# Optimization experiments

Hardware: AMD Instinct MI355X
Metric: run time of the kernel (lower is better)

## Reference

```python
import jax, jax.numpy as jnp
import numpy as np

# LLaMA-style decoder config (shrunken for reference): L layers, hidden D, H heads,
# SwiGLU width F, vocab V, LoRA rank R.
B, S, D, H, F, V, L, R = 2, 512, 1024, 16, 4096, 32000, 2, 16
DH = D // H
LORA_ALPHA = 32.0
EPS = 1e-5
ROPE_THETA = 10000.0


def setup_inputs() -> dict:
    key = jax.random.key(0)
    ks = iter(jax.random.split(key, 40))
    def n(shape, std=0.02):
        return jax.random.normal(next(ks), shape, jnp.float32) * std
    return {
        "input_ids": jax.random.randint(next(ks), (B, S), 0, V),
        "attention_mask": jnp.ones((B, S), jnp.int32),
        "embed": n((V, D)),
        "ln1": jnp.ones((L, D), jnp.float32),
        "ln2": jnp.ones((L, D), jnp.float32),
        "wq": n((L, D, D)), "aq": n((L, D, R)), "bq": n((L, R, D), 0.01),
        "wk": n((L, D, D)), "ak": n((L, D, R)), "bk": n((L, R, D), 0.01),
        "wv": n((L, D, D)), "av": n((L, D, R)), "bv": n((L, R, D), 0.01),
        "wo": n((L, D, D)), "ao": n((L, D, R)), "bo": n((L, R, D), 0.01),
        "wg": n((L, D, F)), "ag": n((L, D, R)), "bg": n((L, R, F), 0.01),
        "wu": n((L, D, F)), "au": n((L, D, R)), "bu": n((L, R, F), 0.01),
        "wd": n((L, F, D)), "ad": n((L, F, R)), "bd": n((L, R, D), 0.01),
        "final_ln": jnp.ones((D,), jnp.float32),
        "lm_head_w": n((D, V)),
        "value_w": n((D, 1)),
        "value_b": jnp.zeros((1,), jnp.float32),
    }


def _rmsnorm(x, w):
    return x * jax.lax.rsqrt(jnp.mean(x * x, axis=-1, keepdims=True) + EPS) * w


def _lin_lora(x, w, a, b):
    # base matmul + low-rank LoRA update scaled by alpha/r (dropout=eval/off)
    return x @ w + ((x @ a) @ b) * (LORA_ALPHA / R)


def _rope_cache(seq_len):
    half = DH // 2
    inv = 1.0 / (ROPE_THETA ** (jnp.arange(half, dtype=jnp.float32) / half))
    ang = jnp.arange(seq_len, dtype=jnp.float32)[:, None] * inv  # [S, half]
    ang = jnp.concatenate([ang, ang], axis=-1)                   # [S, DH]
    return jnp.cos(ang), jnp.sin(ang)


def _apply_rope(x, cos, sin):  # x: [B,S,H,DH]
    h = DH // 2
    rot = jnp.concatenate([-x[..., h:], x[..., :h]], axis=-1)
    return x * cos[None, :, None, :] + rot * sin[None, :, None, :]


def reference(input_ids, attention_mask, embed, ln1, ln2,
              wq, aq, bq, wk, ak, bk, wv, av, bv, wo, ao, bo,
              wg, ag, bg, wu, au, bu, wd, ad, bd,
              final_ln, lm_head_w, value_w, value_b):
    h = embed[input_ids]  # [B,S,D]
    cos, sin = _rope_cache(S)
    causal = jnp.tril(jnp.ones((S, S), bool))
    keep = causal[None, None, :, :] & (attention_mask[:, None, None, :] > 0)
    bias = jnp.where(keep, 0.0, -1e9)  # [B,1,S,S]
    scale = 1.0 / jnp.sqrt(jnp.float32(DH))

    for i in range(L):
        # --- self-attention block ---
        x = _rmsnorm(h, ln1[i])
        q = _lin_lora(x, wq[i], aq[i], bq[i]).reshape(B, S, H, DH)
        k = _lin_lora(x, wk[i], ak[i], bk[i]).reshape(B, S, H, DH)
        v = _lin_lora(x, wv[i], av[i], bv[i]).reshape(B, S, H, DH)
        q = _apply_rope(q, cos, sin)
        k = _apply_rope(k, cos, sin)
        scores = jnp.einsum("bqhd,bkhd->bhqk", q, k) * scale + bias
        attn = jax.nn.softmax(scores, axis=-1)
        o = jnp.einsum("bhqk,bkhd->bqhd", attn, v).reshape(B, S, D)
        h = h + _lin_lora(o, wo[i], ao[i], bo[i])
        # --- SwiGLU MLP block ---
        x = _rmsnorm(h, ln2[i])
        g = jax.nn.silu(_lin_lora(x, wg[i], ag[i], bg[i]))
        u = _lin_lora(x, wu[i], au[i], bu[i])
        h = h + _lin_lora(g * u, wd[i], ad[i], bd[i])

    h = _rmsnorm(h, final_ln)          # HF hidden_states[-1] is post final norm
    logits = h @ lm_head_w             # [B,S,V]
    values = (h @ value_w)[..., 0] + value_b[0]  # [B,S] (squeeze(-1))
    return logits, values
```

## Files before the change

kernel.cpp:

```cpp
#include <hip/hip_runtime.h>
#include <math.h>

constexpr int B = 2, S = 512, D = 1024, H = 16, F = 4096, V = 32000, L = 2, R = 16, DH = 64;
constexpr int BS = B * S;
constexpr float LORA_SCALE = 2.0f;
constexpr float EPS = 1e-5f;
constexpr int RS_QKV = 3 * D;
constexpr int RS_GU  = 2 * F;

typedef __attribute__((ext_vector_type(8))) __bf16 bf16x8;
typedef __attribute__((ext_vector_type(4))) float f32x4;

__device__ __forceinline__ unsigned short f2bf(float f) {
  unsigned u = __builtin_bit_cast(unsigned, f);
  unsigned r = (u + 0x7FFFu + ((u >> 16) & 1u)) >> 16;
  return (unsigned short)r;
}
__device__ __forceinline__ float bf2f(unsigned short us) {
  return __builtin_bit_cast(float, (unsigned)us << 16);
}
__device__ __forceinline__ void load_lds16(const void* g, void* l) {
  __builtin_amdgcn_global_load_lds((const __attribute__((address_space(1))) void*)g,
                                   (__attribute__((address_space(3))) void*)l, 16, 0, 0);
}

struct Ptr3 { const float* p[3]; };

__global__ void rope_cache_kernel(float* __restrict__ cosb, float* __restrict__ sinb) {
  int s = blockIdx.x, j = threadIdx.x;
  float inv = __expf(-(float)j * (9.210340371976184f / 32.0f));
  float ang = (float)s * inv;
  float c = cosf(ang), sn = sinf(ang);
  cosb[s * DH + j] = c;  cosb[s * DH + j + 32] = c;
  sinb[s * DH + j] = sn; sinb[s * DH + j + 32] = sn;
}

__global__ void embed_kernel(const int* __restrict__ ids, const float* __restrict__ emb,
                             float* __restrict__ h) {
  int row = blockIdx.x, t = threadIdx.x;
  int id = ids[row];
  ((float4*)(h + (size_t)row * D))[t] = ((const float4*)(emb + (size_t)id * D))[t];
}

__global__ void rmsnorm_value_kernel(const float* __restrict__ x, const float* __restrict__ w,
                                     const float* __restrict__ vw, const float* __restrict__ vb,
                                     unsigned short* __restrict__ y, float* __restrict__ values) {
  int row = blockIdx.x, t = threadIdx.x;
  float4 xv = ((const float4*)(x + (size_t)row * D))[t];
  float ss = xv.x * xv.x + xv.y * xv.y + xv.z * xv.z + xv.w * xv.w;
  __shared__ float red[256];
  red[t] = ss; __syncthreads();
  for (int s2 = 128; s2; s2 >>= 1) { if (t < s2) red[t] += red[t + s2]; __syncthreads(); }
  float rinv = rsqrtf(red[0] * (1.0f / D) + EPS);
  float4 wv = ((const float4*)w)[t];
  float4 nx;
  nx.x = xv.x * rinv * wv.x; nx.y = xv.y * rinv * wv.y;
  nx.z = xv.z * rinv * wv.z; nx.w = xv.w * rinv * wv.w;
  ushort4 o;
  o.x = f2bf(nx.x); o.y = f2bf(nx.y); o.z = f2bf(nx.z); o.w = f2bf(nx.w);
  ((ushort4*)(y + (size_t)row * D))[t] = o;
  float4 vv = ((const float4*)vw)[t];
  float vd = nx.x * vv.x + nx.y * vv.y + nx.z * vv.z + nx.w * vv.w;
  __syncthreads();
  red[t] = vd; __syncthreads();
  for (int s2 = 128; s2; s2 >>= 1) { if (t < s2) red[t] += red[t + s2]; __syncthreads(); }
  if (t == 0) values[row] = red[0] + vb[0];
}

template <int NA>
__global__ void rms_lora_kernel(const float* __restrict__ hp, const float* __restrict__ w,
                                Ptr3 ap, unsigned short* __restrict__ xbf,
                                unsigned short* __restrict__ t2e) {
  int row = blockIdx.x, t = threadIdx.x;
  int lane = t & 63;
  __shared__ float xs[D];
  __shared__ float red[256];
  float4 xv = ((const float4*)(hp + (size_t)row * D))[t];
  float ss = xv.x * xv.x + xv.y * xv.y + xv.z * xv.z + xv.w * xv.w;
  red[t] = ss; __syncthreads();
  for (int s2 = 128; s2; s2 >>= 1) { if (t < s2) red[t] += red[t + s2]; __syncthreads(); }
  float rinv = rsqrtf(red[0] * (1.0f / D) + EPS);
  float4 wv = ((const float4*)w)[t];
  float4 nx;
  nx.x = xv.x * rinv * wv.x; nx.y = xv.y * rinv * wv.y;
  nx.z = xv.z * rinv * wv.z; nx.w = xv.w * rinv * wv.w;
  xs[t * 4 + 0] = nx.x; xs[t * 4 + 1] = nx.y; xs[t * 4 + 2] = nx.z; xs[t * 4 + 3] = nx.w;
  ushort4 o;
  o.x = f2bf(nx.x); o.y = f2bf(nx.y); o.z = f2bf(nx.z); o.w = f2bf(nx.w);
  ((ushort4*)(xbf + (size_t)row * D))[t] = o;
  if (t >= NA * 16 && t < 64) t2e[(size_t)row * 64 + t] = 0;
  __syncthreads();
  int n = t & 15, g = t >> 4;
#pragma unroll
  for (int ad = 0; ad < NA; ++ad) {
    const float* a = ap.p[ad];
    float s = 0.0f;
    for (int k = g; k < D; k += 16) s = fmaf(xs[k], a[k * 16 + n], s);
    s += __shfl_xor(s, 16);
    s += __shfl_xor(s, 32);
    if (lane < 16) red[(t >> 6) * 16 + n] = s;
    __syncthreads();
    if (t < 16) t2e[(size_t)row * 64 + ad * 16 + t] =
        f2bf(LORA_SCALE * (red[t] + red[t + 16] + red[t + 32] + red[t + 48]));
    if (ad + 1 < NA) __syncthreads();
  }
}

__global__ void lora_o_kernel(const unsigned short* __restrict__ xb, const float* __restrict__ a,
                              unsigned short* __restrict__ t2e) {
  int row = blockIdx.x, t = threadIdx.x;
  int lane = t & 63;
  __shared__ float xs[D];
  __shared__ float red[64];
  for (int k = t; k < D; k += 256) xs[k] = bf2f(xb[(size_t)row * D + k]);
  if (t >= 16 && t < 64) t2e[(size_t)row * 64 + t] = 0;
  __syncthreads();
  int n = t & 15, g = t >> 4;
  float s = 0.0f;
  for (int k = g; k < D; k += 16) s = fmaf(xs[k], a[k * 16 + n], s);
  s += __shfl_xor(s, 16);
  s += __shfl_xor(s, 32);
  if (lane < 16) red[(t >> 6) * 16 + n] = s;
  __syncthreads();
  if (t < 16) t2e[(size_t)row * 64 + t] =
      f2bf(LORA_SCALE * (red[t] + red[t + 16] + red[t + 32] + red[t + 48]));
}

__global__ void silu_lora_kernel(const unsigned short* __restrict__ gub, const float* __restrict__ a,
                                 unsigned short* __restrict__ gbf, unsigned short* __restrict__ t2e) {
  int row = blockIdx.x, t = threadIdx.x;
  int lane = t & 63;
  __shared__ float xs[F];
  __shared__ float red[64];
#pragma unroll
  for (int i2 = 0; i2 < 2; ++i2) {
    int idx = i2 * 256 + t;
    uint4 gv = ((const uint4*)(gub + (size_t)row * RS_GU))[idx];
    uint4 uv = ((const uint4*)(gub + (size_t)row * RS_GU + F))[idx];
    const unsigned* gw = (const unsigned*)&gv;
    const unsigned* uw = (const unsigned*)&uv;
    unsigned short go[8];
#pragma unroll
    for (int q = 0; q < 4; ++q) {
      float g0 = bf2f((unsigned short)(gw[q] & 0xffff)), g1 = bf2f((unsigned short)(gw[q] >> 16));
      float u0 = bf2f((unsigned short)(uw[q] & 0xffff)), u1 = bf2f((unsigned short)(uw[q] >> 16));
      float r0 = g0 / (1.0f + __expf(-g0)) * u0;
      float r1 = g1 / (1.0f + __expf(-g1)) * u1;
      xs[idx * 8 + q * 2] = r0; xs[idx * 8 + q * 2 + 1] = r1;
      go[q * 2] = f2bf(r0); go[q * 2 + 1] = f2bf(r1);
    }
    *(uint4*)(gbf + (size_t)row * F + idx * 8) = *(const uint4*)go;
  }
  if (t >= 16 && t < 64) t2e[(size_t)row * 64 + t] = 0;
  __syncthreads();
  int n = t & 15, g = t >> 4;
  float s = 0.0f;
  for (int k = g; k < F; k += 16) s = fmaf(xs[k], a[k * 16 + n], s);
  s += __shfl_xor(s, 16);
  s += __shfl_xor(s, 32);
  if (lane < 16) red[(t >> 6) * 16 + n] = s;
  __syncthreads();
  if (t < 16) t2e[(size_t)row * 64 + t] =
      f2bf(LORA_SCALE * (red[t] + red[t + 16] + red[t + 32] + red[t + 48]));
}

struct BD { const float* p0; const float* p1; const float* p2;
            unsigned short* dst; int NA; int logW; int nelem; };
struct BDs { BD d[8]; };
__global__ void bext_many_kernel(BDs da) {
  int gid = blockIdx.x * 256 + threadIdx.x;
  int di = 0;
  while (gid >= da.d[di].nelem) { gid -= da.d[di].nelem; ++di; }
  const BD dd = da.d[di];
  int n = gid >> 6, kk = gid & 63;
  int W = 1 << dd.logW;
  int sel = n >> dd.logW;
  const float* bp = (sel == 0) ? dd.p0 : (sel == 1) ? dd.p1 : dd.p2;
  float v = 0.0f;
  if ((kk >> 4) == sel && sel < dd.NA)
    v = bp[(size_t)(kk & 15) * W + (n & (W - 1))];
  dd.dst[(size_t)n * 64 + kk] = f2bf(v);
}

struct TD { const float* src; unsigned short* dst; int K; int N; int nblk; };
struct TDs { TD d[15]; };
__global__ __launch_bounds__(256) void transpose_many_kernel(TDs da) {
  __shared__ unsigned short tile[64 * 264];
  int bid = blockIdx.x;
  int di = 0;
  while (bid >= da.d[di].nblk) { bid -= da.d[di].nblk; ++di; }
  const TD dd = da.d[di];
  int nbx = dd.N >> 6;
  int n0 = (bid % nbx) * 64, k0 = (bid / nbx) * 256;
  int t = threadIdx.x;
  int rr = t >> 4, c4 = (t & 15) << 2;
  float4 v[16];
#pragma unroll
  for (int i = 0; i < 16; ++i)
    v[i] = *(const float4*)(dd.src + (size_t)(k0 + i * 16 + rr) * dd.N + n0 + c4);
#pragma unroll
  for (int i = 0; i < 16; ++i) {
    int k = i * 16 + rr;
#pragma unroll
    for (int j = 0; j < 4; ++j) {
      int n = c4 + j;
      float e = (j == 0) ? v[i].x : (j == 1) ? v[i].y : (j == 2) ? v[i].z : v[i].w;
      tile[n * 264 + (k ^ ((n & 3) << 3))] = f2bf(e);
    }
  }
  __syncthreads();
#pragma unroll
  for (int i = 0; i < 8; ++i) {
    int flat = i * 256 + t;
    int n = flat >> 5, cw = flat & 31;
    int kb = (cw * 8) ^ ((n & 3) << 3);
    *(uint4*)(dd.dst + (size_t)(n0 + n) * dd.K + k0 + cw * 8) =
        *(const uint4*)(tile + n * 264 + kb);
  }
}

template <int BN, bool ACC, bool EXT, int OM>
__global__ __launch_bounds__(256) void gemm_bf16_kernel(
    const unsigned short* __restrict__ A, const unsigned short* __restrict__ Bt,
    void* __restrict__ Cp, int M, int N, int K,
    const unsigned short* __restrict__ Ae, const unsigned short* __restrict__ Be,
    const float* __restrict__ cosb, const float* __restrict__ sinb) {
  constexpr int WM = (BN == 128) ? 2 : 4;
  constexpr int RW = 128 / WM;
  constexpr int MI = RW / 16;
  constexpr int BCH = BN / 32;
  __shared__ __align__(16) unsigned short As[2][128 * 64];
  __shared__ __align__(16) unsigned short Bs[2][BN * 64];
  int t = threadIdx.x;
  int lane = t & 63, wave = t >> 6;
  int wr = (BN == 128) ? (wave >> 1) : wave;
  int wc = (BN == 128) ? (wave & 1) : 0;
  int MT = gridDim.y, NT = gridDim.x;
  int nwg = MT * NT;
  int orig = blockIdx.y * NT + blockIdx.x;
  int qq = nwg >> 3, rr8 = nwg & 7;
  int xcd = orig & 7, pos = orig >> 3;
  int wg = (xcd < rr8) ? (xcd * (qq + 1) + pos) : (rr8 * (qq + 1) + (xcd - rr8) * qq + pos);
  int m0 = (wg % MT) * 128, n0 = (wg / MT) * BN;
  int fr = lane & 15, fq = lane >> 4;
  int xorv = fr & 7;
  f32x4 acc[MI][4] = {};
  int kIters = K / 64;
  int nIters = EXT ? kIters + 1 : kIters;

  auto STAGE = [&](int it, int buf) {
    bool ext = EXT && (it == kIters);
    int k0 = it * 64;
#pragma unroll
    for (int c = 0; c < 4; ++c) {
      int i = c * 256 + t;
      int row = i >> 3, c8 = i & 7;
      int sc = (c8 ^ (row & 7)) * 8;
      const unsigned short* src = ext ? (Ae + (size_t)(m0 + row) * 64 + sc)
                                      : (A + (size_t)(m0 + row) * K + k0 + sc);
      load_lds16(src, &As[buf][i * 8]);
    }
#pragma unroll
    for (int c = 0; c < BCH; ++c) {
      int i = c * 256 + t;
      int row = i >> 3, c8 = i & 7;
      int sc = (c8 ^ (row & 7)) * 8;
      const unsigned short* src = ext ? (Be + (size_t)(n0 + row) * 64 + sc)
                                      : (Bt + (size_t)(n0 + row) * K + k0 + sc);
      load_lds16(src, &Bs[buf][i * 8]);
    }
  };

  STAGE(0, 0);
  if (nIters > 1) STAGE(1, 1);
  int cur = 0;
  for (int it = 0; it < nIters; ++it) {
    if (it + 1 < nIters) {
      if constexpr (BN == 128) asm volatile("s_waitcnt vmcnt(8)" ::: "memory");
      else                     asm volatile("s_waitcnt vmcnt(6)" ::: "memory");
    } else {
      asm volatile("s_waitcnt vmcnt(0)" ::: "memory");
    }
    __builtin_amdgcn_s_barrier();
#pragma unroll
    for (int kk = 0; kk < 2; ++kk) {
      bf16x8 af[MI], bfr[4];
#pragma unroll
      for (int mi = 0; mi < MI; ++mi)
        af[mi] = *(const bf16x8*)(&As[cur][(wr * RW + mi * 16 + fr) * 64 + (((kk * 4 + fq) ^ xorv) << 3)]);
#pragma unroll
      for (int ni = 0; ni < 4; ++ni)
        bfr[ni] = *(const bf16x8*)(&Bs[cur][(wc * 64 + ni * 16 + fr) * 64 + (((kk * 4 + fq) ^ xorv) << 3)]);
#pragma unroll
      for (int mi = 0; mi < MI; ++mi)
#pragma unroll
        for (int ni = 0; ni < 4; ++ni)
          acc[mi][ni] = __builtin_amdgcn_mfma_f32_16x16x32_bf16(af[mi], bfr[ni], acc[mi][ni], 0, 0, 0);
    }
    __builtin_amdgcn_s_barrier();
    if (it + 2 < nIters) STAGE(it + 2, cur);
    cur ^= 1;
  }
  if constexpr (OM == 0) {
    float* C = (float*)Cp;
#pragma unroll
    for (int mi = 0; mi < MI; ++mi)
#pragma unroll
      for (int ni = 0; ni < 4; ++ni)
#pragma unroll
        for (int j = 0; j < 4; ++j) {
          int r = m0 + wr * RW + mi * 16 + fq * 4 + j;
          int cl = n0 + wc * 64 + ni * 16 + fr;
          size_t idx = (size_t)r * N + cl;
          float v = acc[mi][ni][j];
          C[idx] = ACC ? C[idx] + v : v;
        }
  } else {
    unsigned short* Cb = (unsigned short*)Cp;
#pragma unroll
    for (int mi = 0; mi < MI; ++mi)
#pragma unroll
      for (int j = 0; j < 4; ++j) {
        int r = m0 + wr * RW + mi * 16 + fq * 4 + j;
        if constexpr (OM == 2) {
          int s = r & (S - 1);
#pragma unroll
          for (int ni = 0; ni < 2; ++ni) {
            int cl0 = n0 + wc * 64 + ni * 16 + fr;
            int cl1 = cl0 + 32;
            float x0 = acc[mi][ni][j], x1 = acc[mi][ni + 2][j];
            if (cl0 < 2 * D) {
              int dh = cl0 & 63;
              float cz = cosb[s * DH + dh], sz = sinb[s * DH + dh];
              float y0 = x0 * cz - x1 * sz;
              float y1 = x1 * cz + x0 * sz;
              x0 = y0; x1 = y1;
            }
            Cb[(size_t)r * N + cl0] = f2bf(x0);
            Cb[(size_t)r * N + cl1] = f2bf(x1);
          }
        } else {
#pragma unroll
          for (int ni = 0; ni < 4; ++ni) {
            int cl = n0 + wc * 64 + ni * 16 + fr;
            Cb[(size_t)r * N + cl] = f2bf(acc[mi][ni][j]);
          }
        }
      }
  }
}

__global__ __launch_bounds__(512) void gemm256_kernel(
    const unsigned short* __restrict__ A, const unsigned short* __restrict__ Bt,
    float* __restrict__ C, int M, int N, int K) {
  __shared__ __align__(16) unsigned short As[2][256 * 64];
  __shared__ __align__(16) unsigned short Bs[2][256 * 64];
  int t = threadIdx.x;
  int lane = t & 63, wave = t >> 6;
  int wr = wave >> 2, wc = wave & 3;
  int MT = gridDim.y, NT = gridDim.x;
  int nwg = MT * NT;
  int orig = blockIdx.y * NT + blockIdx.x;
  int qq = nwg >> 3, rr8 = nwg & 7;
  int xcd = orig & 7, pos = orig >> 3;
  int wg = (xcd < rr8) ? (xcd * (qq + 1) + pos) : (rr8 * (qq + 1) + (xcd - rr8) * qq + pos);
  int m0 = (wg % MT) * 256, n0 = (wg / MT) * 256;
  int fr = lane & 15, fq = lane >> 4;
  int xorv = fr & 7;
  f32x4 acc[8][4] = {};
  int kIters = K / 64;

  auto STAGE = [&](int it, int buf) {
    int k0 = it * 64;
#pragma unroll
    for (int c = 0; c < 4; ++c) {
      int i = c * 512 + t;
      int row = i >> 3, c8 = i & 7;
      int sc = (c8 ^ (row & 7)) * 8;
      load_lds16(A + (size_t)(m0 + row) * K + k0 + sc, &As[buf][i * 8]);
    }
#pragma unroll
    for (int c = 0; c < 4; ++c) {
      int i = c * 512 + t;
      int row = i >> 3, c8 = i & 7;
      int sc = (c8 ^ (row & 7)) * 8;
      load_lds16(Bt + (size_t)(n0 + row) * K + k0 + sc, &Bs[buf][i * 8]);
    }
  };

  STAGE(0, 0);
  if (kIters > 1) STAGE(1, 1);
  int cur = 0;
  for (int it = 0; it < kIters; ++it) {
    if (it + 1 < kIters) asm volatile("s_waitcnt vmcnt(8)" ::: "memory");
    else                 asm volatile("s_waitcnt vmcnt(0)" ::: "memory");
    __builtin_amdgcn_s_barrier();
    __builtin_amdgcn_s_setprio(1);
#pragma unroll
    for (int kk = 0; kk < 2; ++kk) {
      bf16x8 af[8], bfr[4];
#pragma unroll
      for (int mi = 0; mi < 8; ++mi)
        af[mi] = *(const bf16x8*)(&As[cur][(wr * 128 + mi * 16 + fr) * 64 + (((kk * 4 + fq) ^ xorv) << 3)]);
#pragma unroll
      for (int ni = 0; ni < 4; ++ni)
        bfr[ni] = *(const bf16x8*)(&Bs[cur][(wc * 64 + ni * 16 + fr) * 64 + (((kk * 4 + fq) ^ xorv) << 3)]);
#pragma unroll
      for (int mi = 0; mi < 8; ++mi)
#pragma unroll
        for (int ni = 0; ni < 4; ++ni)
          acc[mi][ni] = __builtin_amdgcn_mfma_f32_16x16x32_bf16(af[mi], bfr[ni], acc[mi][ni], 0, 0, 0);
    }
    __builtin_amdgcn_s_setprio(0);
    __builtin_amdgcn_s_barrier();
    if (it + 2 < kIters) STAGE(it + 2, cur);
    cur ^= 1;
  }
#pragma unroll
  for (int mi = 0; mi < 8; ++mi)
#pragma unroll
    for (int ni = 0; ni < 4; ++ni)
#pragma unroll
      for (int j = 0; j < 4; ++j) {
        int r = m0 + wr * 128 + mi * 16 + fq * 4 + j;
        int cl = n0 + wc * 64 + ni * 16 + fr;
        C[(size_t)r * N + cl] = acc[mi][ni][j];
      }
}

__global__ __launch_bounds__(256) void attn_mfma_kernel(
    const unsigned short* __restrict__ qkvb, const int* __restrict__ amask,
    unsigned short* __restrict__ o) {
  __shared__ unsigned short Qs[64 * 72];
  __shared__ unsigned short Ks[64 * 72];
  __shared__ unsigned short Vt[64 * 72];
  __shared__ unsigned short Ps[4][16 * 72];
  __shared__ float msk[64];
  int bid = blockIdx.x;
  int qt = bid & 7, hh = (bid >> 3) & (H - 1), b = bid >> 7;
  int t = threadIdx.x;
  int lane = t & 63, w = t >> 6;
  int fr = lane & 15, fq = lane >> 4;
  size_t rowbase = (size_t)b * S;
  int q0 = qt * 64;
  const float scale = 0.125f;
#pragma unroll
  for (int c = 0; c < 2; ++c) {
    int i = c * 256 + t;
    int row = i >> 3, ch = i & 7;
    *(uint4*)(Qs + row * 72 + ch * 8) =
        *(const uint4*)(qkvb + (rowbase + q0 + row) * RS_QKV + hh * DH + ch * 8);
  }
  f32x4 oacc[4] = {};
  float m_old[4] = {-1e30f, -1e30f, -1e30f, -1e30f};
  float l[4] = {};
  int qbase = q0 + w * 16;
  for (int kt = 0; kt <= qt; ++kt) {
    int kk0 = kt * 64;
#pragma unroll
    for (int c = 0; c < 2; ++c) {
      int i = c * 256 + t;
      int row = i >> 3, ch = i & 7;
      uint4 kv = *(const uint4*)(qkvb + (rowbase + kk0 + row) * RS_QKV + D + hh * DH + ch * 8);
      *(uint4*)(Ks + row * 72 + ch * 8) = kv;
    }
#pragma unroll
    for (int c = 0; c < 2; ++c) {
      int idx = c * 256 + t;
      int rp = idx >> 4, dg = idx & 15;
      const unsigned short* vsrc = qkvb + (rowbase + kk0 + rp * 2) * RS_QKV + 2 * D + hh * DH + dg * 4;
      uint2 lo = *(const uint2*)vsrc;
      uint2 hi = *(const uint2*)(vsrc + RS_QKV);
      const unsigned short* ls = (const unsigned short*)&lo;
      const unsigned short* hs = (const unsigned short*)&hi;
#pragma unroll
      for (int q = 0; q < 4; ++q) {
        unsigned pk = (unsigned)ls[q] | ((unsigned)hs[q] << 16);
        *(unsigned*)(Vt + (dg * 4 + q) * 72 + rp * 2) = pk;
      }
    }
    if (t < 64) msk[t] = (amask[b * S + kk0 + t] > 0) ? 0.0f : -1e9f;
    __syncthreads();
    bf16x8 aq[2];
    aq[0] = *(const bf16x8*)(Qs + (w * 16 + fr) * 72 + fq * 8);
    aq[1] = *(const bf16x8*)(Qs + (w * 16 + fr) * 72 + 32 + fq * 8);
    f32x4 sacc[4];
#pragma unroll
    for (int ct = 0; ct < 4; ++ct) {
      bf16x8 bk0 = *(const bf16x8*)(Ks + (ct * 16 + fr) * 72 + fq * 8);
      bf16x8 bk1 = *(const bf16x8*)(Ks + (ct * 16 + fr) * 72 + 32 + fq * 8);
      f32x4 z = {};
      z = __builtin_amdgcn_mfma_f32_16x16x32_bf16(aq[0], bk0, z, 0, 0, 0);
      sacc[ct] = __builtin_amdgcn_mfma_f32_16x16x32_bf16(aq[1], bk1, z, 0, 0, 0);
    }
    float sv[4][4];
#pragma unroll
    for (int ct = 0; ct < 4; ++ct) {
      int kg = kk0 + ct * 16 + fr;
      float mk = msk[ct * 16 + fr];
#pragma unroll
      for (int j = 0; j < 4; ++j) {
        int qg = qbase + fq * 4 + j;
        float s = sacc[ct][j] * scale + mk;
        sv[ct][j] = (kg > qg) ? -1e9f : s;
      }
    }
    float mnew[4], f[4], rsum[4];
#pragma unroll
    for (int j = 0; j < 4; ++j) {
      float mt = fmaxf(fmaxf(sv[0][j], sv[1][j]), fmaxf(sv[2][j], sv[3][j]));
      for (int off = 1; off < 16; off <<= 1) mt = fmaxf(mt, __shfl_xor(mt, off));
      mnew[j] = fmaxf(m_old[j], mt);
      f[j] = __expf(m_old[j] - mnew[j]);
      float rs = 0.0f;
#pragma unroll
      for (int ct = 0; ct < 4; ++ct) {
        float e = __expf(sv[ct][j] - mnew[j]);
        sv[ct][j] = e;
        rs += e;
      }
      for (int off = 1; off < 16; off <<= 1) rs += __shfl_xor(rs, off);
      rsum[j] = rs;
      l[j] = l[j] * f[j] + rsum[j];
      m_old[j] = mnew[j];
#pragma unroll
      for (int dt = 0; dt < 4; ++dt) oacc[dt][j] *= f[j];
    }
#pragma unroll
    for (int ct = 0; ct < 4; ++ct)
#pragma unroll
      for (int j = 0; j < 4; ++j)
        Ps[w][(fq * 4 + j) * 72 + ct * 16 + fr] = f2bf(sv[ct][j]);
    __syncthreads();
    bf16x8 pa[2];
    pa[0] = *(const bf16x8*)(&Ps[w][fr * 72 + fq * 8]);
    pa[1] = *(const bf16x8*)(&Ps[w][fr * 72 + 32 + fq * 8]);
#pragma unroll
    for (int dt = 0; dt < 4; ++dt) {
      bf16x8 vb0 = *(const bf16x8*)(Vt + (dt * 16 + fr) * 72 + fq * 8);
      bf16x8 vb1 = *(const bf16x8*)(Vt + (dt * 16 + fr) * 72 + 32 + fq * 8);
      oacc[dt] = __builtin_amdgcn_mfma_f32_16x16x32_bf16(pa[0], vb0, oacc[dt], 0, 0, 0);
      oacc[dt] = __builtin_amdgcn_mfma_f32_16x16x32_bf16(pa[1], vb1, oacc[dt], 0, 0, 0);
    }
    __syncthreads();
  }
#pragma unroll
  for (int j = 0; j < 4; ++j) {
    float rinv = 1.0f / l[j];
    int qrow = qbase + fq * 4 + j;
#pragma unroll
    for (int dt = 0; dt < 4; ++dt)
      o[(rowbase + qrow) * D + hh * DH + dt * 16 + fr] = f2bf(oacc[dt][j] * rinv);
  }
}

extern "C" void kernel_launch(void* const* d_in, const int* in_sizes, int n_in,
                              void* d_out, int out_size, void* d_ws, size_t ws_size,
                              hipStream_t stream) {
  const int*   ids     = (const int*)d_in[0];
  const int*   amask   = (const int*)d_in[1];
  const float* emb     = (const float*)d_in[2];
  const float* ln1     = (const float*)d_in[3];
  const float* ln2     = (const float*)d_in[4];
  const float* wq = (const float*)d_in[5],  *aq = (const float*)d_in[6],  *bq = (const float*)d_in[7];
  const float* wk = (const float*)d_in[8],  *ak = (const float*)d_in[9],  *bk = (const float*)d_in[10];
  const float* wv = (const float*)d_in[11], *av = (const float*)d_in[12], *bv = (const float*)d_in[13];
  const float* wo = (const float*)d_in[14], *ao = (const float*)d_in[15], *bo = (const float*)d_in[16];
  const float* wg = (const float*)d_in[17], *ag = (const float*)d_in[18], *bg = (const float*)d_in[19];
  const float* wu = (const float*)d_in[20], *au = (const float*)d_in[21], *bu = (const float*)d_in[22];
  const float* wd = (const float*)d_in[23], *ad = (const float*)d_in[24], *bd = (const float*)d_in[25];
  const float* final_ln  = (const float*)d_in[26];
  const float* lm_head_w = (const float*)d_in[27];
  const float* value_w   = (const float*)d_in[28];
  const float* value_b   = (const float*)d_in[29];

  float* out    = (float*)d_out;
  float* logits = out;
  float* values = out + (size_t)BS * V;

  float* Wf = (float*)d_ws;
  float* cosb = Wf; Wf += S * DH;
  float* sinb = Wf; Wf += S * DH;
  float* h    = Wf; Wf += (size_t)BS * D;
  unsigned short* Wb = (unsigned short*)Wf;
  unsigned short* x_bf  = Wb; Wb += (size_t)BS * D;
  unsigned short* t2e   = Wb; Wb += (size_t)BS * 64;
  unsigned short* qg    = Wb; Wb += (size_t)BS * F;
  unsigned short* gu_bf = Wb; Wb += (size_t)BS * RS_GU;
  unsigned short* wqkvT = Wb; Wb += (size_t)L * 3 * D * D;
  unsigned short* woT   = Wb; Wb += (size_t)L * D * D;
  unsigned short* wguT  = Wb; Wb += (size_t)L * 2 * D * F;
  unsigned short* wdT   = Wb; Wb += (size_t)L * F * D;
  unsigned short* lmT   = Wb; Wb += (size_t)D * V;
  unsigned short* beQKV = Wb; Wb += (size_t)L * 3 * D * 64;
  unsigned short* beO   = Wb; Wb += (size_t)L * D * 64;
  unsigned short* beGU  = Wb; Wb += (size_t)L * 2 * F * 64;
  unsigned short* beD   = Wb; Wb += (size_t)L * D * 64;
  unsigned short* qkv_bf = qg;
  unsigned short* gbf    = qg;
  unsigned short* obf    = gu_bf;

  TDs td; int tblocks = 0; int di = 0;
  auto addT = [&](const float* s, unsigned short* dp, int K_, int N_) {
    td.d[di] = {s, dp, K_, N_, (K_ / 256) * (N_ / 64)};
    tblocks += td.d[di].nblk; ++di;
  };
  for (int l = 0; l < L; ++l) {
    size_t DD = (size_t)D * D, DF = (size_t)D * F;
    addT(wq + l * DD, wqkvT + (size_t)l * 3 * DD, D, D);
    addT(wk + l * DD, wqkvT + (size_t)l * 3 * DD + DD, D, D);
    addT(wv + l * DD, wqkvT + (size_t)l * 3 * DD + 2 * DD, D, D);
    addT(wo + l * DD, woT + l * DD, D, D);
    addT(wg + l * DF, wguT + (size_t)l * 2 * DF, D, F);
    addT(wu + l * DF, wguT + (size_t)l * 2 * DF + DF, D, F);
    addT(wd + l * DF, wdT + l * DF, F, D);
  }
  addT(lm_head_w, lmT, D, V);
  transpose_many_kernel<<<dim3(tblocks), 256, 0, stream>>>(td);

  BDs bd2; int belems = 0; di = 0;
  auto addB = [&](const float* p0, const float* p1, const float* p2,
                  unsigned short* dst, int NA, int logW, int N_) {
    bd2.d[di] = {p0, p1, p2, dst, NA, logW, N_ * 64};
    belems += N_ * 64; ++di;
  };
  for (int l = 0; l < L; ++l) {
    size_t oRD = (size_t)l * R * D, oRF = (size_t)l * R * F;
    addB(bq + oRD, bk + oRD, bv + oRD, beQKV + (size_t)l * 3 * D * 64, 3, 10, 3 * D);
    addB(bo + oRD, nullptr, nullptr,   beO   + (size_t)l * D * 64,     1, 10, D);
    addB(bg + oRF, bu + oRF, nullptr,  beGU  + (size_t)l * 2 * F * 64, 2, 12, 2 * F);
    addB(bd + oRD, nullptr, nullptr,   beD   + (size_t)l * D * 64,     1, 10, D);
  }
  bext_many_kernel<<<dim3(belems / 256), 256, 0, stream>>>(bd2);

  rope_cache_kernel<<<dim3(S), dim3(32), 0, stream>>>(cosb, sinb);
  embed_kernel<<<dim3(BS), dim3(256), 0, stream>>>(ids, emb, h);

  for (int l = 0; l < L; ++l) {
    size_t DD = (size_t)D * D, DF = (size_t)D * F;
    size_t oDR = (size_t)l * D * R, oFR = (size_t)l * F * R;

    { Ptr3 ap = {{aq + oDR, ak + oDR, av + oDR}};
      rms_lora_kernel<3><<<dim3(BS), 256, 0, stream>>>(h, ln1 + (size_t)l * D, ap, x_bf, t2e); }
    gemm_bf16_kernel<128, false, true, 2><<<dim3(3 * D / 128, BS / 128), 256, 0, stream>>>(
        x_bf, wqkvT + (size_t)l * 3 * DD, qkv_bf, BS, 3 * D, D,
        t2e, beQKV + (size_t)l * 3 * D * 64, cosb, sinb);

    attn_mfma_kernel<<<dim3(B * H * (S / 64)), 256, 0, stream>>>(qkv_bf, amask, obf);

    lora_o_kernel<<<dim3(BS), 256, 0, stream>>>(obf, ao + oDR, t2e);
    gemm_bf16_kernel<64, true, true, 0><<<dim3(D / 64, BS / 128), 256, 0, stream>>>(
        obf, woT + l * DD, h, BS, D, D, t2e, beO + (size_t)l * D * 64, nullptr, nullptr);

    { Ptr3 ap = {{ag + oDR, au + oDR, nullptr}};
      rms_lora_kernel<2><<<dim3(BS), 256, 0, stream>>>(h, ln2 + (size_t)l * D, ap, x_bf, t2e); }
    gemm_bf16_kernel<128, false, true, 1><<<dim3(2 * F / 128, BS / 128), 256, 0, stream>>>(
        x_bf, wguT + (size_t)l * 2 * DF, gu_bf, BS, 2 * F, D,
        t2e, beGU + (size_t)l * 2 * F * 64, nullptr, nullptr);

    silu_lora_kernel<<<dim3(BS), 256, 0, stream>>>(gu_bf, ad + oFR, gbf, t2e);

    gemm_bf16_kernel<64, true, true, 0><<<dim3(D / 64, BS / 128), 256, 0, stream>>>(
        gbf, wdT + l * DF, h, BS, D, F, t2e, beD + (size_t)l * D * 64, nullptr, nullptr);
  }

  rmsnorm_value_kernel<<<dim3(BS), 256, 0, stream>>>(h, final_ln, value_w, value_b, x_bf, values);
  gemm256_kernel<<<dim3(V / 256, BS / 256), 512, 0, stream>>>(x_bf, lmT, logits, BS, V, D);
}
```

Measured before the change: 1.006 ms.

## Add BM template parameter for smaller GEMM tiles and rewrite weight transpose via LDS

Adds a BM template parameter to the bf16 GEMM so the QKV, O-proj and down-proj GEMMs use 64-row tiles. This doubles the workgroup count on the small 1024-row problems to fill more CUs. The weight transpose kernel now loads fp32 tiles straight into swizzled LDS with global_load_lds, on a 128-row tile, and converts to bf16 on the read side. The trade-off is less data reuse per tile in the GEMMs and more, smaller transpose blocks.

Result: faster. 958.3 us (-4.7%).

```diff
diff --git a/kernel.cpp b/kernel.cpp
--- a/kernel.cpp
+++ b/kernel.cpp
@@ -185,66 +185,68 @@
 struct TD { const float* src; unsigned short* dst; int K; int N; int nblk; };
 struct TDs { TD d[15]; };
 __global__ __launch_bounds__(256) void transpose_many_kernel(TDs da) {
-  __shared__ unsigned short tile[64 * 264];
+  __shared__ __align__(16) float tile[128 * 64];
   int bid = blockIdx.x;
   int di = 0;
   while (bid >= da.d[di].nblk) { bid -= da.d[di].nblk; ++di; }
   const TD dd = da.d[di];
   int nbx = dd.N >> 6;
-  int n0 = (bid % nbx) * 64, k0 = (bid / nbx) * 256;
+  int n0 = (bid % nbx) * 64, k0 = (bid / nbx) * 128;
   int t = threadIdx.x;
-  int rr = t >> 4, c4 = (t & 15) << 2;
-  float4 v[16];
-#pragma unroll
-  for (int i = 0; i < 16; ++i)
-    v[i] = *(const float4*)(dd.src + (size_t)(k0 + i * 16 + rr) * dd.N + n0 + c4);
-#pragma unroll
-  for (int i = 0; i < 16; ++i) {
-    int k = i * 16 + rr;
-#pragma unroll
-    for (int j = 0; j < 4; ++j) {
-      int n = c4 + j;
-      float e = (j == 0) ? v[i].x : (j == 1) ? v[i].y : (j == 2) ? v[i].z : v[i].w;
-      tile[n * 264 + (k ^ ((n & 3) << 3))] = f2bf(e);
-    }
-  }
-  __syncthreads();
 #pragma unroll
   for (int i = 0; i < 8; ++i) {
-    int flat = i * 256 + t;
-    int n = flat >> 5, cw = flat & 31;
-    int kb = (cw * 8) ^ ((n & 3) << 3);
-    *(uint4*)(dd.dst + (size_t)(n0 + n) * dd.K + k0 + cw * 8) =
-        *(const uint4*)(tile + n * 264 + kb);
-  }
-}
-
-template <int BN, bool ACC, bool EXT, int OM>
+    int s = i * 256 + t;
+    int k = s >> 4, cp = s & 15;
+    int c = cp ^ (k >> 3);
+    load_lds16(dd.src + (size_t)(k0 + k) * dd.N + n0 + c * 4, &tile[s * 4]);
+  }
+  asm volatile("s_waitcnt vmcnt(0)" ::: "memory");
+  __builtin_amdgcn_s_barrier();
+#pragma unroll
+  for (int j2 = 0; j2 < 4; ++j2) {
+    int flat = j2 * 256 + t;
+    int n = flat >> 4, kc = flat & 15;
+    int cs = ((n >> 2) ^ kc) << 2;
+    unsigned short o8[8];
+#pragma unroll
+    for (int q = 0; q < 8; ++q) {
+      int k = kc * 8 + q;
+      o8[q] = f2bf(tile[k * 64 + cs + (n & 3)]);
+    }
+    *(uint4*)(dd.dst + (size_t)(n0 + n) * dd.K + k0 + kc * 8) = *(const uint4*)o8;
+  }
+}
+
+template <int BM, int BN, bool ACC, bool EXT, int OM>
 __global__ __launch_bounds__(256) void gemm_bf16_kernel(
     const unsigned short* __restrict__ A, const unsigned short* __restrict__ Bt,
     void* __restrict__ Cp, int M, int N, int K,
     const unsigned short* __restrict__ Ae, const unsigned short* __restrict__ Be,
     const float* __restrict__ cosb, const float* __restrict__ sinb) {
-  constexpr int WM = (BN == 128) ? 2 : 4;
-  constexpr int RW = 128 / WM;
+  constexpr int WC = (BM == 64 || BN == 128) ? 2 : 1;
+  constexpr int WR = 4 / WC;
+  constexpr int RW = BM / WR;
   constexpr int MI = RW / 16;
+  constexpr int CN = BN / WC;
+  constexpr int NI = CN / 16;
+  constexpr int ACH = BM / 32;
   constexpr int BCH = BN / 32;
-  __shared__ __align__(16) unsigned short As[2][128 * 64];
+  constexpr int NLOADS = ACH + BCH;
+  __shared__ __align__(16) unsigned short As[2][BM * 64];
   __shared__ __align__(16) unsigned short Bs[2][BN * 64];
   int t = threadIdx.x;
   int lane = t & 63, wave = t >> 6;
-  int wr = (BN == 128) ? (wave >> 1) : wave;
-  int wc = (BN == 128) ? (wave & 1) : 0;
+  int wr = wave / WC, wc = wave % WC;
   int MT = gridDim.y, NT = gridDim.x;
   int nwg = MT * NT;
   int orig = blockIdx.y * NT + blockIdx.x;
   int qq = nwg >> 3, rr8 = nwg & 7;
   int xcd = orig & 7, pos = orig >> 3;
   int wg = (xcd < rr8) ? (xcd * (qq + 1) + pos) : (rr8 * (qq + 1) + (xcd - rr8) * qq + pos);
-  int m0 = (wg % MT) * 128, n0 = (wg / MT) * BN;
+  int m0 = (wg % MT) * BM, n0 = (wg / MT) * BN;
   int fr = lane & 15, fq = lane >> 4;
   int xorv = fr & 7;
-  f32x4 acc[MI][4] = {};
+  f32x4 acc[MI][NI] = {};
   int kIters = K / 64;
   int nIters = EXT ? kIters + 1 : kIters;
 
@@ -252,7 +254,7 @@
     bool ext = EXT && (it == kIters);
     int k0 = it * 64;
 #pragma unroll
-    for (int c = 0; c < 4; ++c) {
+    for (int c = 0; c < ACH; ++c) {
       int i = c * 256 + t;
       int row = i >> 3, c8 = i & 7;
       int sc = (c8 ^ (row & 7)) * 8;
@@ -276,25 +278,26 @@
   int cur = 0;
   for (int it = 0; it < nIters; ++it) {
     if (it + 1 < nIters) {
-      if constexpr (BN == 128) asm volatile("s_waitcnt vmcnt(8)" ::: "memory");
-      else                     asm volatile("s_waitcnt vmcnt(6)" ::: "memory");
+      if constexpr (NLOADS == 8)      asm volatile("s_waitcnt vmcnt(8)" ::: "memory");
+      else if constexpr (NLOADS == 6) asm volatile("s_waitcnt vmcnt(6)" ::: "memory");
+      else                            asm volatile("s_waitcnt vmcnt(4)" ::: "memory");
     } else {
       asm volatile("s_waitcnt vmcnt(0)" ::: "memory");
     }
     __builtin_amdgcn_s_barrier();
 #pragma unroll
     for (int kk = 0; kk < 2; ++kk) {
-      bf16x8 af[MI], bfr[4];
+      bf16x8 af[MI], bfr[NI];
 #pragma unroll
       for (int mi = 0; mi < MI; ++mi)
         af[mi] = *(const bf16x8*)(&As[cur][(wr * RW + mi * 16 + fr) * 64 + (((kk * 4 + fq) ^ xorv) << 3)]);
 #pragma unroll
-      for (int ni = 0; ni < 4; ++ni)
-        bfr[ni] = *(const bf16x8*)(&Bs[cur][(wc * 64 + ni * 16 + fr) * 64 + (((kk * 4 + fq) ^ xorv) << 3)]);
+      for (int ni = 0; ni < NI; ++ni)
+        bfr[ni] = *(const bf16x8*)(&Bs[cur][(wc * CN + ni * 16 + fr) * 64 + (((kk * 4 + fq) ^ xorv) << 3)]);
 #pragma unroll
       for (int mi = 0; mi < MI; ++mi)
 #pragma unroll
-        for (int ni = 0; ni < 4; ++ni)
+        for (int ni = 0; ni < NI; ++ni)
           acc[mi][ni] = __builtin_amdgcn_mfma_f32_16x16x32_bf16(af[mi], bfr[ni], acc[mi][ni], 0, 0, 0);
     }
     __builtin_amdgcn_s_barrier();
@@ -306,11 +309,11 @@
 #pragma unroll
     for (int mi = 0; mi < MI; ++mi)
 #pragma unroll
-      for (int ni = 0; ni < 4; ++ni)
+      for (int ni = 0; ni < NI; ++ni)
 #pragma unroll
         for (int j = 0; j < 4; ++j) {
           int r = m0 + wr * RW + mi * 16 + fq * 4 + j;
-          int cl = n0 + wc * 64 + ni * 16 + fr;
+          int cl = n0 + wc * CN + ni * 16 + fr;
           size_t idx = (size_t)r * N + cl;
           float v = acc[mi][ni][j];
           C[idx] = ACC ? C[idx] + v : v;
@@ -326,7 +329,7 @@
           int s = r & (S - 1);
 #pragma unroll
           for (int ni = 0; ni < 2; ++ni) {
-            int cl0 = n0 + wc * 64 + ni * 16 + fr;
+            int cl0 = n0 + wc * CN + ni * 16 + fr;
             int cl1 = cl0 + 32;
             float x0 = acc[mi][ni][j], x1 = acc[mi][ni + 2][j];
             if (cl0 < 2 * D) {
@@ -341,8 +344,8 @@
           }
         } else {
 #pragma unroll
-          for (int ni = 0; ni < 4; ++ni) {
-            int cl = n0 + wc * 64 + ni * 16 + fr;
+          for (int ni = 0; ni < NI; ++ni) {
+            int cl = n0 + wc * CN + ni * 16 + fr;
             Cb[(size_t)r * N + cl] = f2bf(acc[mi][ni][j]);
           }
         }
@@ -602,7 +605,7 @@
 
   TDs td; int tblocks = 0; int di = 0;
   auto addT = [&](const float* s, unsigned short* dp, int K_, int N_) {
-    td.d[di] = {s, dp, K_, N_, (K_ / 256) * (N_ / 64)};
+    td.d[di] = {s, dp, K_, N_, (K_ / 128) * (N_ / 64)};
     tblocks += td.d[di].nblk; ++di;
   };
   for (int l = 0; l < L; ++l) {
@@ -642,25 +645,25 @@
 
     { Ptr3 ap = {{aq + oDR, ak + oDR, av + oDR}};
       rms_lora_kernel<3><<<dim3(BS), 256, 0, stream>>>(h, ln1 + (size_t)l * D, ap, x_bf, t2e); }
-    gemm_bf16_kernel<128, false, true, 2><<<dim3(3 * D / 128, BS / 128), 256, 0, stream>>>(
+    gemm_bf16_kernel<64, 128, false, true, 2><<<dim3(3 * D / 128, BS / 64), 256, 0, stream>>>(
         x_bf, wqkvT + (size_t)l * 3 * DD, qkv_bf, BS, 3 * D, D,
         t2e, beQKV + (size_t)l * 3 * D * 64, cosb, sinb);
 
     attn_mfma_kernel<<<dim3(B * H * (S / 64)), 256, 0, stream>>>(qkv_bf, amask, obf);
 
     lora_o_kernel<<<dim3(BS), 256, 0, stream>>>(obf, ao + oDR, t2e);
-    gemm_bf16_kernel<64, true, true, 0><<<dim3(D / 64, BS / 128), 256, 0, stream>>>(
+    gemm_bf16_kernel<64, 64, true, true, 0><<<dim3(D / 64, BS / 64), 256, 0, stream>>>(
         obf, woT + l * DD, h, BS, D, D, t2e, beO + (size_t)l * D * 64, nullptr, nullptr);
 
     { Ptr3 ap = {{ag + oDR, au + oDR, nullptr}};
       rms_lora_kernel<2><<<dim3(BS), 256, 0, stream>>>(h, ln2 + (size_t)l * D, ap, x_bf, t2e); }
-    gemm_bf16_kernel<128, false, true, 1><<<dim3(2 * F / 128, BS / 128), 256, 0, stream>>>(
+    gemm_bf16_kernel<128, 128, false, true, 1><<<dim3(2 * F / 128, BS / 128), 256, 0, stream>>>(
         x_bf, wguT + (size_t)l * 2 * DF, gu_bf, BS, 2 * F, D,
         t2e, beGU + (size_t)l * 2 * F * 64, nullptr, nullptr);
 
     silu_lora_kernel<<<dim3(BS), 256, 0, stream>>>(gu_bf, ad + oFR, gbf, t2e);
 
-    gemm_bf16_kernel<64, true, true, 0><<<dim3(D / 64, BS / 128), 256, 0, stream>>>(
+    gemm_bf16_kernel<64, 64, true, true, 0><<<dim3(D / 64, BS / 64), 256, 0, stream>>>(
         gbf, wdT + l * DF, h, BS, D, F, t2e, beD + (size_t)l * D * 64, nullptr, nullptr);
   }
 
```
